# Kernel tuning notes

Hardware: AMD Instinct MI355X
Metric: run time of the kernel (lower is better)

## Reference

```python
import jax, jax.numpy as jnp
import numpy as np

ALPHA = 4.0   # spikingjelly surrogate.Sigmoid default alpha
TAU = 2.0
HEADS = 8

@jax.custom_vjp
def spike_fn(x):
    return (x >= 0).astype(x.dtype)

def _spike_fwd(x):
    return spike_fn(x), x

def _spike_bwd(x, g):
    s = jax.nn.sigmoid(ALPHA * x)
    return (g * ALPHA * s * (1.0 - s),)

spike_fn.defvjp(_spike_fwd, _spike_bwd)

def lif(x, v_th=1.0):
    """Multi-step LIF over leading time axis. Hard reset to 0, detach_reset."""
    def step(v, xt):
        v = v + (xt - v) / TAU
        s = spike_fn(v - v_th)
        v = v * (1.0 - jax.lax.stop_gradient(s))
        return v, s
    _, spikes = jax.lax.scan(step, jnp.zeros_like(x[0]), x)
    return spikes

def conv1x1(x, w, b=None):
    # x: (T,B,C,H,W), w: (O,C) -> (T,B,O,H,W)
    y = jnp.einsum('tbchw,oc->tbohw', x, w)
    if b is not None:
        y = y + b[None, None, :, None, None]
    return y

def bn(x, gamma, beta, mean, var, eps=1e-5):
    inv = gamma / jnp.sqrt(var + eps)
    shift = beta - mean * inv
    return x * inv[None, None, :, None, None] + shift[None, None, :, None, None]

def setup_inputs() -> dict:
    key = jax.random.key(0)
    T, B, C, H, W = 4, 16, 512, 16, 16
    ks = jax.random.split(key, 24)
    def w(k):
        return jax.random.normal(k, (C, C), jnp.float32) * (1.0 / np.sqrt(C))
    def bn_params(k0, k1):
        g = 1.0 + 0.1 * jax.random.normal(k0, (C,), jnp.float32)
        b = 0.1 * jax.random.normal(k1, (C,), jnp.float32)
        m = 0.1 * jax.random.normal(jax.random.fold_in(k0, 7), (C,), jnp.float32)
        v = jax.random.uniform(jax.random.fold_in(k1, 7), (C,), jnp.float32, 0.5, 1.5)
        return g, b, m, v
    x = jax.random.normal(ks[0], (T, B, C, H, W), jnp.float32)
    q_g, q_b, q_m, q_v = bn_params(ks[4], ks[5])
    k_g, k_b, k_m, k_v = bn_params(ks[6], ks[7])
    v_g, v_b, v_m, v_v = bn_params(ks[8], ks[9])
    p_g, p_b2, p_m, p_v = bn_params(ks[10], ks[11])
    return {
        'x': x,
        'q_w': w(ks[1]), 'q_g': q_g, 'q_b': q_b, 'q_m': q_m, 'q_v': q_v,
        'k_w': w(ks[2]), 'k_g': k_g, 'k_b': k_b, 'k_m': k_m, 'k_v': k_v,
        'v_w': w(ks[3]), 'v_g': v_g, 'v_b': v_b, 'v_m': v_m, 'v_v': v_v,
        'proj_w': w(ks[12]),
        'proj_b': 0.1 * jax.random.normal(ks[13], (C,), jnp.float32),
        'p_g': p_g, 'p_b2': p_b2, 'p_m': p_m, 'p_v': p_v,
    }

def reference(x, q_w, q_g, q_b, q_m, q_v, k_w, k_g, k_b, k_m, k_v,
              v_w, v_g, v_b, v_m, v_v, proj_w, proj_b, p_g, p_b2, p_m, p_v):
    T, B, C, H, W = x.shape
    d = C // HEADS
    N = H * W
    identity = x
    xs = lif(x)  # shortcut_lif

    def to_heads(y):
        # (T,B,C,H,W) -> flatten(3) -> (T,B,C,N) -> (T,B,N,C) -> (T,B,N,h,d) -> (T,B,h,N,d)
        return y.reshape(T, B, C, N).transpose(0, 1, 3, 2).reshape(T, B, N, HEADS, d).transpose(0, 1, 3, 2, 4)

    q = to_heads(lif(bn(conv1x1(xs, q_w), q_g, q_b, q_m, q_v)))
    k = to_heads(lif(bn(conv1x1(xs, k_w), k_g, k_b, k_m, k_v)))
    v = to_heads(lif(bn(conv1x1(xs, v_w), v_g, v_b, v_m, v_v)))

    kv = (k * v).sum(axis=3, keepdims=True)        # (T,B,h,1,d) linear spike attention
    kv = lif(kv, v_th=0.5)                         # talking_heads_lif (conv1d never applied in source forward)
    attn = q * kv                                  # (T,B,h,N,d)

    y = attn.transpose(0, 1, 2, 4, 3).reshape(T, B, C, H, W)
    y = bn(conv1x1(y, proj_w, proj_b), p_g, p_b2, p_m, p_v)
    return y + identity
```

## Files before the change

### kernel.cpp

```cpp
#include <hip/hip_runtime.h>


#define T_  4
#define B_  16
#define C_  512
#define N_  256
#define O3_ 1536
#define EPS_ 1e-5f

typedef unsigned int uint32;

__global__ void k0_prep(const float* __restrict__ qw, const float* __restrict__ kw,
                        const float* __restrict__ vw, const float* __restrict__ pw,
                        const float* qg,const float* qb,const float* qm,const float* qv,
                        const float* kg,const float* kb,const float* km,const float* kvr,
                        const float* vg,const float* vb,const float* vm,const float* vv,
                        const float* pg,const float* pb2,const float* pm,const float* pv,
                        const float* projb,
                        float* __restrict__ wqkv_t, float* __restrict__ pwt,
                        float* __restrict__ bnc){
    __shared__ float tile[64 * 65];
    int bx = blockIdx.x, tid = threadIdx.x;
    if (bx < 256) {
        const float* src; float* dst; int ocol;
        int tl;
        if (bx < 192) { int g = bx / 64; tl = bx % 64;
            src = (g == 0) ? qw : (g == 1) ? kw : vw;
            dst = wqkv_t; ocol = g * 512;
        } else { tl = bx - 192; src = pw; dst = pwt; ocol = 0; }
        int o0 = (tl >> 3) * 64, c0 = (tl & 7) * 64;
        int dstride = (bx < 192) ? O3_ : C_;
        #pragma unroll
        for (int i = 0; i < 16; i++) {
            int idx = i * 256 + tid;
            int cl = idx & 63, ol = idx >> 6;
            tile[ol * 65 + cl] = src[(size_t)(o0 + ol) * C_ + c0 + cl];
        }
        __syncthreads();
        #pragma unroll
        for (int i = 0; i < 16; i++) {
            int idx = i * 256 + tid;
            int ol = idx & 63, cl = idx >> 6;
            dst[(size_t)(c0 + cl) * dstride + ocol + o0 + ol] = tile[ol * 65 + cl];
        }
    } else {
        int ch = (bx - 256) * 256 + tid;
        if (ch < C_) {
            {   float inv = qg[ch] / sqrtf(qv[ch] + EPS_);
                bnc[ch] = inv;            bnc[512 + ch]  = qb[ch] - qm[ch] * inv; }
            {   float inv = kg[ch] / sqrtf(kvr[ch] + EPS_);
                bnc[1024 + ch] = inv;     bnc[1536 + ch] = kb[ch] - km[ch] * inv; }
            {   float inv = vg[ch] / sqrtf(vv[ch] + EPS_);
                bnc[2048 + ch] = inv;     bnc[2560 + ch] = vb[ch] - vm[ch] * inv; }
            {   float inv = pg[ch] / sqrtf(pv[ch] + EPS_);
                float shift = pb2[ch] - pm[ch] * inv;
                bnc[3072 + ch] = inv;     bnc[3584 + ch] = projb[ch] * inv + shift; }
        }
    }
}

__global__ void k1_lif_x(const float* __restrict__ x, unsigned char* __restrict__ xs_mask){
    __shared__ unsigned char sm[64 * 68];
    int b = blockIdx.x, c0 = blockIdx.y * 64, n0 = blockIdx.z * 64;
    int tid = threadIdx.x;
    #pragma unroll
    for (int i = 0; i < 16; i++) {
        int idx = i * 256 + tid;
        int nl = idx & 63, cl = idx >> 6;
        const float* xp = x + ((size_t)b * C_ + c0 + cl) * N_ + n0 + nl;
        float v = 0.f; unsigned m = 0;
        #pragma unroll
        for (int t = 0; t < T_; t++) {
            float xt = xp[(size_t)t * B_ * C_ * N_];
            v = v + (xt - v) * 0.5f;
            if (v - 1.0f >= 0.f) { m |= 1u << t; v = 0.f; }
        }
        sm[cl * 68 + nl] = (unsigned char)m;
    }
    __syncthreads();
    #pragma unroll
    for (int i = 0; i < 16; i++) {
        int idx = i * 256 + tid;
        int cl = idx & 63, nl = idx >> 6;
        xs_mask[((size_t)b * N_ + n0 + nl) * C_ + c0 + cl] = sm[cl * 68 + nl];
    }
}

__global__ __launch_bounds__(384) void
k2_qkv(const unsigned char* __restrict__ xs_mask,
       const float* __restrict__ wqkv_t,
       const float* __restrict__ bnc,
       unsigned char* __restrict__ q_mask,
       unsigned char* __restrict__ kvand_mask){
    __shared__ uint32 smask[128];
    __shared__ uint32 scnt;
    __shared__ uint32 slist[512];
    int n = blockIdx.x, b = blockIdx.y, tid = threadIdx.x;
    size_t colbase = ((size_t)b * N_ + n) * C_;
    if (tid < 128) smask[tid] = reinterpret_cast<const uint32*>(xs_mask + colbase)[tid];
    if (tid == 0) scnt = 0;
    __syncthreads();
    if (tid < 256) {
        const unsigned char* smb = (const unsigned char*)smask;
        #pragma unroll
        for (int h = 0; h < 2; h++) {
            int c = tid + (h << 8);
            unsigned m = smb[c];
            if (m) { unsigned p = atomicAdd(&scnt, 1u); slist[p] = (unsigned)c | (m << 16); }
        }
    }
    __syncthreads();
    int cnt = scnt;

    int g = tid >> 7;
    float acc[4][4];
    #pragma unroll
    for (int t = 0; t < 4; t++)
        #pragma unroll
        for (int i = 0; i < 4; i++) acc[t][i] = 0.f;

#define ACC4(t, w_) { acc[t][0]+=w_.x; acc[t][1]+=w_.y; acc[t][2]+=w_.z; acc[t][3]+=w_.w; }
    int j = 0;
    for (; j + 4 <= cnt; j += 4) {
        unsigned e0 = __builtin_amdgcn_readfirstlane(slist[j]);
        unsigned e1 = __builtin_amdgcn_readfirstlane(slist[j + 1]);
        unsigned e2 = __builtin_amdgcn_readfirstlane(slist[j + 2]);
        unsigned e3 = __builtin_amdgcn_readfirstlane(slist[j + 3]);
        float4 w0 = reinterpret_cast<const float4*>(wqkv_t + (size_t)(e0 & 0xffffu) * O3_)[tid];
        float4 w1 = reinterpret_cast<const float4*>(wqkv_t + (size_t)(e1 & 0xffffu) * O3_)[tid];
        float4 w2 = reinterpret_cast<const float4*>(wqkv_t + (size_t)(e2 & 0xffffu) * O3_)[tid];
        float4 w3 = reinterpret_cast<const float4*>(wqkv_t + (size_t)(e3 & 0xffffu) * O3_)[tid];
        unsigned m0 = e0 >> 16, m1 = e1 >> 16, m2 = e2 >> 16, m3 = e3 >> 16;
        if (m0 & 1u) ACC4(0, w0)  if (m0 & 2u) ACC4(1, w0)
        if (m0 & 4u) ACC4(2, w0)  if (m0 & 8u) ACC4(3, w0)
        if (m1 & 1u) ACC4(0, w1)  if (m1 & 2u) ACC4(1, w1)
        if (m1 & 4u) ACC4(2, w1)  if (m1 & 8u) ACC4(3, w1)
        if (m2 & 1u) ACC4(0, w2)  if (m2 & 2u) ACC4(1, w2)
        if (m2 & 4u) ACC4(2, w2)  if (m2 & 8u) ACC4(3, w2)
        if (m3 & 1u) ACC4(0, w3)  if (m3 & 2u) ACC4(1, w3)
        if (m3 & 4u) ACC4(2, w3)  if (m3 & 8u) ACC4(3, w3)
    }
    for (; j < cnt; j++) {
        unsigned e0 = __builtin_amdgcn_readfirstlane(slist[j]);
        float4 w0 = reinterpret_cast<const float4*>(wqkv_t + (size_t)(e0 & 0xffffu) * O3_)[tid];
        unsigned m0 = e0 >> 16;
        if (m0 & 1u) ACC4(0, w0)  if (m0 & 2u) ACC4(1, w0)
        if (m0 & 4u) ACC4(2, w0)  if (m0 & 8u) ACC4(3, w0)
    }
#undef ACC4

    int chb = (tid & 127) * 4;
    unsigned packed = 0;
    #pragma unroll
    for (int i = 0; i < 4; i++) {
        int ch = chb + i;
        float inv = bnc[g * 1024 + ch];
        float sh  = bnc[g * 1024 + 512 + ch];
        float v = 0.f; unsigned bits = 0;
        #pragma unroll
        for (int t = 0; t < 4; t++) {
            float pre = acc[t][i] * inv + sh;
            v = v + (pre - v) * 0.5f;
            if (v - 1.0f >= 0.f) { bits |= 1u << t; v = 0.f; }
        }
        packed |= bits << (8 * i);
    }
    if (g == 0)      reinterpret_cast<uint32*>(q_mask + colbase)[tid] = packed;
    else if (g == 1) smask[tid - 128] = packed;
    __syncthreads();
    if (g == 2) {
        unsigned kb = smask[tid - 256];
        reinterpret_cast<uint32*>(kvand_mask + colbase)[tid - 256] = packed & kb;
    }
}

__global__ void k3_kv(const unsigned char* __restrict__ kvand_mask,
                      unsigned char* __restrict__ kvs_mask){
    int c = blockIdx.x * 256 + threadIdx.x;
    int b = blockIdx.y;
    int cnt[4] = {0, 0, 0, 0};
    const unsigned char* p = kvand_mask + (size_t)b * N_ * C_ + c;
    for (int n = 0; n < N_; n++) {
        unsigned m = p[(size_t)n * C_];
        #pragma unroll
        for (int t = 0; t < 4; t++) cnt[t] += (m >> t) & 1;
    }
    float v = 0.f; unsigned bits = 0;
    #pragma unroll
    for (int t = 0; t < 4; t++) {
        float kvf = (float)cnt[t];
        v = v + (kvf - v) * 0.5f;
        if (v - 0.5f >= 0.f) { bits |= 1u << t; v = 0.f; }
    }
    kvs_mask[b * C_ + c] = (unsigned char)bits;
}

__global__ __launch_bounds__(128) void
k4_attn_proj(const unsigned char* __restrict__ q_mask,
             const unsigned char* __restrict__ kvs_mask,
             const float* __restrict__ pwt,
             const float* __restrict__ bnc,
             float* __restrict__ y_t){
    __shared__ uint32 smask[128];
    __shared__ uint32 scnt;
    __shared__ uint32 slist[512];
    int n = blockIdx.x, b = blockIdx.y, tid = threadIdx.x;
    size_t colbase = ((size_t)b * N_ + n) * C_;
    {
        uint32 qm = reinterpret_cast<const uint32*>(q_mask + colbase)[tid];
        uint32 kv = reinterpret_cast<const uint32*>(kvs_mask + (size_t)b * C_)[tid];
        smask[tid] = qm & kv;
    }
    if (tid == 0) scnt = 0;
    __syncthreads();
    {
        const unsigned char* smb = (const unsigned char*)smask;
        #pragma unroll
        for (int h = 0; h < 4; h++) {
            int c = tid * 4 + h;
            unsigned m = smb[c];
            if (m) { unsigned p = atomicAdd(&scnt, 1u); slist[p] = (unsigned)c | (m << 16); }
        }
    }
    __syncthreads();
    int cnt = scnt;

    float acc[4][4];
    #pragma unroll
    for (int t = 0; t < 4; t++)
        #pragma unroll
        for (int i = 0; i < 4; i++) acc[t][i] = 0.f;

#define ACC4(t, w_) { acc[t][0]+=w_.x; acc[t][1]+=w_.y; acc[t][2]+=w_.z; acc[t][3]+=w_.w; }
    int j = 0;
    for (; j + 4 <= cnt; j += 4) {
        unsigned e0 = __builtin_amdgcn_readfirstlane(slist[j]);
        unsigned e1 = __builtin_amdgcn_readfirstlane(slist[j + 1]);
        unsigned e2 = __builtin_amdgcn_readfirstlane(slist[j + 2]);
        unsigned e3 = __builtin_amdgcn_readfirstlane(slist[j + 3]);
        float4 w0 = reinterpret_cast<const float4*>(pwt + (size_t)(e0 & 0xffffu) * C_)[tid];
        float4 w1 = reinterpret_cast<const float4*>(pwt + (size_t)(e1 & 0xffffu) * C_)[tid];
        float4 w2 = reinterpret_cast<const float4*>(pwt + (size_t)(e2 & 0xffffu) * C_)[tid];
        float4 w3 = reinterpret_cast<const float4*>(pwt + (size_t)(e3 & 0xffffu) * C_)[tid];
        unsigned m0 = e0 >> 16, m1 = e1 >> 16, m2 = e2 >> 16, m3 = e3 >> 16;
        if (m0 & 1u) ACC4(0, w0)  if (m0 & 2u) ACC4(1, w0)
        if (m0 & 4u) ACC4(2, w0)  if (m0 & 8u) ACC4(3, w0)
        if (m1 & 1u) ACC4(0, w1)  if (m1 & 2u) ACC4(1, w1)
        if (m1 & 4u) ACC4(2, w1)  if (m1 & 8u) ACC4(3, w1)
        if (m2 & 1u) ACC4(0, w2)  if (m2 & 2u) ACC4(1, w2)
        if (m2 & 4u) ACC4(2, w2)  if (m2 & 8u) ACC4(3, w2)
        if (m3 & 1u) ACC4(0, w3)  if (m3 & 2u) ACC4(1, w3)
        if (m3 & 4u) ACC4(2, w3)  if (m3 & 8u) ACC4(3, w3)
    }
    for (; j < cnt; j++) {
        unsigned e0 = __builtin_amdgcn_readfirstlane(slist[j]);
        float4 w0 = reinterpret_cast<const float4*>(pwt + (size_t)(e0 & 0xffffu) * C_)[tid];
        unsigned m0 = e0 >> 16;
        if (m0 & 1u) ACC4(0, w0)  if (m0 & 2u) ACC4(1, w0)
        if (m0 & 4u) ACC4(2, w0)  if (m0 & 8u) ACC4(3, w0)
    }
#undef ACC4

    float4 inv = reinterpret_cast<const float4*>(bnc + 3072)[tid];
    float4 sh  = reinterpret_cast<const float4*>(bnc + 3584)[tid];
    #pragma unroll
    for (int t = 0; t < 4; t++) {
        float4 y4;
        y4.x = acc[t][0] * inv.x + sh.x;
        y4.y = acc[t][1] * inv.y + sh.y;
        y4.z = acc[t][2] * inv.z + sh.z;
        y4.w = acc[t][3] * inv.w + sh.w;
        reinterpret_cast<float4*>(y_t + (((size_t)t * B_ + b) * N_ + n) * C_)[tid] = y4;
    }
}

__global__ void k5_out(const float* __restrict__ y_t, const float* __restrict__ x,
                       float* __restrict__ out){
    __shared__ float tile[64 * 65];
    int b = blockIdx.x, o0 = blockIdx.y * 64, n0 = blockIdx.z * 64;
    int tid = threadIdx.x;
    for (int t = 0; t < T_; t++) {
        __syncthreads();
        #pragma unroll
        for (int i = 0; i < 16; i++) {
            int idx = i * 256 + tid;
            int ol = idx & 63, nl = idx >> 6;
            tile[ol * 65 + nl] =
                y_t[(((size_t)t * B_ + b) * N_ + n0 + nl) * C_ + o0 + ol];
        }
        __syncthreads();
        #pragma unroll
        for (int i = 0; i < 16; i++) {
            int idx = i * 256 + tid;
            int nl = idx & 63, ol = idx >> 6;
            size_t a = (((size_t)t * B_ + b) * C_ + o0 + ol) * N_ + n0 + nl;
            out[a] = tile[ol * 65 + nl] + x[a];
        }
    }
}

extern "C" void kernel_launch(void* const* d_in, const int* in_sizes, int n_in,
                              void* d_out, int out_size, void* d_ws, size_t ws_size,
                              hipStream_t stream){
    const float* x     = (const float*)d_in[0];
    const float* q_w   = (const float*)d_in[1];
    const float* q_g   = (const float*)d_in[2];
    const float* q_b   = (const float*)d_in[3];
    const float* q_m   = (const float*)d_in[4];
    const float* q_v   = (const float*)d_in[5];
    const float* k_w   = (const float*)d_in[6];
    const float* k_g   = (const float*)d_in[7];
    const float* k_b   = (const float*)d_in[8];
    const float* k_m   = (const float*)d_in[9];
    const float* k_v   = (const float*)d_in[10];
    const float* v_w   = (const float*)d_in[11];
    const float* v_g   = (const float*)d_in[12];
    const float* v_b   = (const float*)d_in[13];
    const float* v_m   = (const float*)d_in[14];
    const float* v_v   = (const float*)d_in[15];
    const float* pr_w  = (const float*)d_in[16];
    const float* pr_b  = (const float*)d_in[17];
    const float* p_g   = (const float*)d_in[18];
    const float* p_b2  = (const float*)d_in[19];
    const float* p_m   = (const float*)d_in[20];
    const float* p_v   = (const float*)d_in[21];
    float* out = (float*)d_out;

    char* ws = (char*)d_ws;
    float* wqkv_t          = (float*)(ws + 0);
    float* pwt             = (float*)(ws + 3145728);
    float* bnc             = (float*)(ws + 4194304);
    unsigned char* xs_mask = (unsigned char*)(ws + 4210688);
    unsigned char* q_mask  = (unsigned char*)(ws + 6307840);
    unsigned char* kvand   = (unsigned char*)(ws + 8404992);
    unsigned char* kvs     = (unsigned char*)(ws + 10502144);
    float* y_t             = (float*)(ws + 10510336);

    hipLaunchKernelGGL(k0_prep, dim3(258), dim3(256), 0, stream,
                       q_w, k_w, v_w, pr_w,
                       q_g,q_b,q_m,q_v, k_g,k_b,k_m,k_v, v_g,v_b,v_m,v_v,
                       p_g,p_b2,p_m,p_v, pr_b, wqkv_t, pwt, bnc);
    hipLaunchKernelGGL(k1_lif_x, dim3(B_, C_/64, N_/64), dim3(256), 0, stream, x, xs_mask);
    hipLaunchKernelGGL(k2_qkv, dim3(N_, B_), dim3(384), 0, stream,
                       xs_mask, wqkv_t, bnc, q_mask, kvand);
    hipLaunchKernelGGL(k3_kv, dim3(2, B_), dim3(256), 0, stream, kvand, kvs);
    hipLaunchKernelGGL(k4_attn_proj, dim3(N_, B_), dim3(128), 0, stream,
                       q_mask, kvs, pwt, bnc, y_t);
    hipLaunchKernelGGL(k5_out, dim3(B_, C_/64, N_/64), dim3(256), 0, stream, y_t, x, out);
}
```

Baseline: 218.2 us.

## Unroll sparse gathers by 8, SWAR-count kv masks, vectorize output transpose

The sparse weight-gather loops in the QKV and projection kernels are unrolled from 4 to 8 entries, putting more global loads in flight per iteration. The kv reduction kernel now reads 32-bit words and counts four channels at once with SWAR byte lanes, splitting the N dimension across two thread halves combined through shared memory. The output transpose-plus-residual kernel uses float4 global loads and stores. The changes add register pressure in the gather loops and cut k3 to 16 blocks, which leaves very little parallelism.

```diff
diff --git a/kernel.cpp b/kernel.cpp
--- a/kernel.cpp
+++ b/kernel.cpp
@@ -120,33 +120,36 @@
         for (int i = 0; i < 4; i++) acc[t][i] = 0.f;
 
 #define ACC4(t, w_) { acc[t][0]+=w_.x; acc[t][1]+=w_.y; acc[t][2]+=w_.z; acc[t][3]+=w_.w; }
+#define K2MASK(u) { unsigned mm = e##u >> 16; \
+        if (mm & 1u) ACC4(0, w##u)  if (mm & 2u) ACC4(1, w##u) \
+        if (mm & 4u) ACC4(2, w##u)  if (mm & 8u) ACC4(3, w##u) }
     int j = 0;
-    for (; j + 4 <= cnt; j += 4) {
-        unsigned e0 = __builtin_amdgcn_readfirstlane(slist[j]);
+    for (; j + 8 <= cnt; j += 8) {
+        unsigned e0 = __builtin_amdgcn_readfirstlane(slist[j + 0]);
         unsigned e1 = __builtin_amdgcn_readfirstlane(slist[j + 1]);
         unsigned e2 = __builtin_amdgcn_readfirstlane(slist[j + 2]);
         unsigned e3 = __builtin_amdgcn_readfirstlane(slist[j + 3]);
+        unsigned e4 = __builtin_amdgcn_readfirstlane(slist[j + 4]);
+        unsigned e5 = __builtin_amdgcn_readfirstlane(slist[j + 5]);
+        unsigned e6 = __builtin_amdgcn_readfirstlane(slist[j + 6]);
+        unsigned e7 = __builtin_amdgcn_readfirstlane(slist[j + 7]);
         float4 w0 = reinterpret_cast<const float4*>(wqkv_t + (size_t)(e0 & 0xffffu) * O3_)[tid];
         float4 w1 = reinterpret_cast<const float4*>(wqkv_t + (size_t)(e1 & 0xffffu) * O3_)[tid];
         float4 w2 = reinterpret_cast<const float4*>(wqkv_t + (size_t)(e2 & 0xffffu) * O3_)[tid];
         float4 w3 = reinterpret_cast<const float4*>(wqkv_t + (size_t)(e3 & 0xffffu) * O3_)[tid];
-        unsigned m0 = e0 >> 16, m1 = e1 >> 16, m2 = e2 >> 16, m3 = e3 >> 16;
-        if (m0 & 1u) ACC4(0, w0)  if (m0 & 2u) ACC4(1, w0)
-        if (m0 & 4u) ACC4(2, w0)  if (m0 & 8u) ACC4(3, w0)
-        if (m1 & 1u) ACC4(0, w1)  if (m1 & 2u) ACC4(1, w1)
-        if (m1 & 4u) ACC4(2, w1)  if (m1 & 8u) ACC4(3, w1)
-        if (m2 & 1u) ACC4(0, w2)  if (m2 & 2u) ACC4(1, w2)
-        if (m2 & 4u) ACC4(2, w2)  if (m2 & 8u) ACC4(3, w2)
-        if (m3 & 1u) ACC4(0, w3)  if (m3 & 2u) ACC4(1, w3)
-        if (m3 & 4u) ACC4(2, w3)  if (m3 & 8u) ACC4(3, w3)
+        float4 w4 = reinterpret_cast<const float4*>(wqkv_t + (size_t)(e4 & 0xffffu) * O3_)[tid];
+        float4 w5 = reinterpret_cast<const float4*>(wqkv_t + (size_t)(e5 & 0xffffu) * O3_)[tid];
+        float4 w6 = reinterpret_cast<const float4*>(wqkv_t + (size_t)(e6 & 0xffffu) * O3_)[tid];
+        float4 w7 = reinterpret_cast<const float4*>(wqkv_t + (size_t)(e7 & 0xffffu) * O3_)[tid];
+        K2MASK(0) K2MASK(1) K2MASK(2) K2MASK(3)
+        K2MASK(4) K2MASK(5) K2MASK(6) K2MASK(7)
     }
     for (; j < cnt; j++) {
         unsigned e0 = __builtin_amdgcn_readfirstlane(slist[j]);
         float4 w0 = reinterpret_cast<const float4*>(wqkv_t + (size_t)(e0 & 0xffffu) * O3_)[tid];
-        unsigned m0 = e0 >> 16;
-        if (m0 & 1u) ACC4(0, w0)  if (m0 & 2u) ACC4(1, w0)
-        if (m0 & 4u) ACC4(2, w0)  if (m0 & 8u) ACC4(3, w0)
-    }
+        K2MASK(0)
+    }
+#undef K2MASK
 #undef ACC4
 
     int chb = (tid & 127) * 4;
@@ -174,25 +177,43 @@
     }
 }
 
-__global__ void k3_kv(const unsigned char* __restrict__ kvand_mask,
+__global__ void k3_kv(const uint32* __restrict__ kvand32,
                       unsigned char* __restrict__ kvs_mask){
-    int c = blockIdx.x * 256 + threadIdx.x;
-    int b = blockIdx.y;
-    int cnt[4] = {0, 0, 0, 0};
-    const unsigned char* p = kvand_mask + (size_t)b * N_ * C_ + c;
-    for (int n = 0; n < N_; n++) {
-        unsigned m = p[(size_t)n * C_];
-        #pragma unroll
-        for (int t = 0; t < 4; t++) cnt[t] += (m >> t) & 1;
-    }
-    float v = 0.f; unsigned bits = 0;
-    #pragma unroll
-    for (int t = 0; t < 4; t++) {
-        float kvf = (float)cnt[t];
-        v = v + (kvf - v) * 0.5f;
-        if (v - 0.5f >= 0.f) { bits |= 1u << t; v = 0.f; }
-    }
-    kvs_mask[b * C_ + c] = (unsigned char)bits;
+    __shared__ uint32 part[4][128];
+    int b = blockIdx.x, tid = threadIdx.x;
+    int c4 = tid & 127, sub = tid >> 7;
+    const uint32* p = kvand32 + (size_t)b * N_ * 128 + (size_t)sub * 128 * 128 + c4;
+    uint32 cnt0 = 0, cnt1 = 0, cnt2 = 0, cnt3 = 0;
+    for (int i = 0; i < 128; i++) {
+        uint32 m = p[(size_t)i * 128];
+        cnt0 +=  m        & 0x01010101u;
+        cnt1 += (m >> 1)  & 0x01010101u;
+        cnt2 += (m >> 2)  & 0x01010101u;
+        cnt3 += (m >> 3)  & 0x01010101u;
+    }
+    if (sub == 1) { part[0][c4] = cnt0; part[1][c4] = cnt1; part[2][c4] = cnt2; part[3][c4] = cnt3; }
+    __syncthreads();
+    if (sub == 0) {
+        uint32 o0 = part[0][c4], o1 = part[1][c4], o2 = part[2][c4], o3 = part[3][c4];
+        unsigned outp = 0;
+        #pragma unroll
+        for (int e = 0; e < 4; e++) {
+            int sh = 8 * e;
+            float cn[4];
+            cn[0] = (float)(int)(((cnt0 >> sh) & 0xffu) + ((o0 >> sh) & 0xffu));
+            cn[1] = (float)(int)(((cnt1 >> sh) & 0xffu) + ((o1 >> sh) & 0xffu));
+            cn[2] = (float)(int)(((cnt2 >> sh) & 0xffu) + ((o2 >> sh) & 0xffu));
+            cn[3] = (float)(int)(((cnt3 >> sh) & 0xffu) + ((o3 >> sh) & 0xffu));
+            float v = 0.f; unsigned bits = 0;
+            #pragma unroll
+            for (int t = 0; t < 4; t++) {
+                v = v + (cn[t] - v) * 0.5f;
+                if (v - 0.5f >= 0.f) { bits |= 1u << t; v = 0.f; }
+            }
+            outp |= bits << sh;
+        }
+        reinterpret_cast<uint32*>(kvs_mask + (size_t)b * C_)[c4] = outp;
+    }
 }
 
 __global__ __launch_bounds__(128) void
@@ -232,33 +253,36 @@
         for (int i = 0; i < 4; i++) acc[t][i] = 0.f;
 
 #define ACC4(t, w_) { acc[t][0]+=w_.x; acc[t][1]+=w_.y; acc[t][2]+=w_.z; acc[t][3]+=w_.w; }
+#define K4MASK(u) { unsigned mm = e##u >> 16; \
+        if (mm & 1u) ACC4(0, w##u)  if (mm & 2u) ACC4(1, w##u) \
+        if (mm & 4u) ACC4(2, w##u)  if (mm & 8u) ACC4(3, w##u) }
     int j = 0;
-    for (; j + 4 <= cnt; j += 4) {
-        unsigned e0 = __builtin_amdgcn_readfirstlane(slist[j]);
+    for (; j + 8 <= cnt; j += 8) {
+        unsigned e0 = __builtin_amdgcn_readfirstlane(slist[j + 0]);
         unsigned e1 = __builtin_amdgcn_readfirstlane(slist[j + 1]);
         unsigned e2 = __builtin_amdgcn_readfirstlane(slist[j + 2]);
         unsigned e3 = __builtin_amdgcn_readfirstlane(slist[j + 3]);
+        unsigned e4 = __builtin_amdgcn_readfirstlane(slist[j + 4]);
+        unsigned e5 = __builtin_amdgcn_readfirstlane(slist[j + 5]);
+        unsigned e6 = __builtin_amdgcn_readfirstlane(slist[j + 6]);
+        unsigned e7 = __builtin_amdgcn_readfirstlane(slist[j + 7]);
         float4 w0 = reinterpret_cast<const float4*>(pwt + (size_t)(e0 & 0xffffu) * C_)[tid];
         float4 w1 = reinterpret_cast<const float4*>(pwt + (size_t)(e1 & 0xffffu) * C_)[tid];
         float4 w2 = reinterpret_cast<const float4*>(pwt + (size_t)(e2 & 0xffffu) * C_)[tid];
         float4 w3 = reinterpret_cast<const float4*>(pwt + (size_t)(e3 & 0xffffu) * C_)[tid];
-        unsigned m0 = e0 >> 16, m1 = e1 >> 16, m2 = e2 >> 16, m3 = e3 >> 16;
-        if (m0 & 1u) ACC4(0, w0)  if (m0 & 2u) ACC4(1, w0)
-        if (m0 & 4u) ACC4(2, w0)  if (m0 & 8u) ACC4(3, w0)
-        if (m1 & 1u) ACC4(0, w1)  if (m1 & 2u) ACC4(1, w1)
-        if (m1 & 4u) ACC4(2, w1)  if (m1 & 8u) ACC4(3, w1)
-        if (m2 & 1u) ACC4(0, w2)  if (m2 & 2u) ACC4(1, w2)
-        if (m2 & 4u) ACC4(2, w2)  if (m2 & 8u) ACC4(3, w2)
-        if (m3 & 1u) ACC4(0, w3)  if (m3 & 2u) ACC4(1, w3)
-        if (m3 & 4u) ACC4(2, w3)  if (m3 & 8u) ACC4(3, w3)
+        float4 w4 = reinterpret_cast<const float4*>(pwt + (size_t)(e4 & 0xffffu) * C_)[tid];
+        float4 w5 = reinterpret_cast<const float4*>(pwt + (size_t)(e5 & 0xffffu) * C_)[tid];
+        float4 w6 = reinterpret_cast<const float4*>(pwt + (size_t)(e6 & 0xffffu) * C_)[tid];
+        float4 w7 = reinterpret_cast<const float4*>(pwt + (size_t)(e7 & 0xffffu) * C_)[tid];
+        K4MASK(0) K4MASK(1) K4MASK(2) K4MASK(3)
+        K4MASK(4) K4MASK(5) K4MASK(6) K4MASK(7)
     }
     for (; j < cnt; j++) {
         unsigned e0 = __builtin_amdgcn_readfirstlane(slist[j]);
         float4 w0 = reinterpret_cast<const float4*>(pwt + (size_t)(e0 & 0xffffu) * C_)[tid];
-        unsigned m0 = e0 >> 16;
-        if (m0 & 1u) ACC4(0, w0)  if (m0 & 2u) ACC4(1, w0)
-        if (m0 & 4u) ACC4(2, w0)  if (m0 & 8u) ACC4(3, w0)
-    }
+        K4MASK(0)
+    }
+#undef K4MASK
 #undef ACC4
 
     float4 inv = reinterpret_cast<const float4*>(bnc + 3072)[tid];
@@ -282,19 +306,29 @@
     for (int t = 0; t < T_; t++) {
         __syncthreads();
         #pragma unroll
-        for (int i = 0; i < 16; i++) {
+        for (int i = 0; i < 4; i++) {
             int idx = i * 256 + tid;
-            int ol = idx & 63, nl = idx >> 6;
-            tile[ol * 65 + nl] =
-                y_t[(((size_t)t * B_ + b) * N_ + n0 + nl) * C_ + o0 + ol];
+            int o4 = idx & 15, nl = idx >> 4;
+            float4 yv = *reinterpret_cast<const float4*>(
+                y_t + (((size_t)t * B_ + b) * N_ + n0 + nl) * C_ + o0 + o4 * 4);
+            tile[(o4 * 4 + 0) * 65 + nl] = yv.x;
+            tile[(o4 * 4 + 1) * 65 + nl] = yv.y;
+            tile[(o4 * 4 + 2) * 65 + nl] = yv.z;
+            tile[(o4 * 4 + 3) * 65 + nl] = yv.w;
         }
         __syncthreads();
         #pragma unroll
-        for (int i = 0; i < 16; i++) {
+        for (int i = 0; i < 4; i++) {
             int idx = i * 256 + tid;
-            int nl = idx & 63, ol = idx >> 6;
-            size_t a = (((size_t)t * B_ + b) * C_ + o0 + ol) * N_ + n0 + nl;
-            out[a] = tile[ol * 65 + nl] + x[a];
+            int n4 = idx & 15, ol = idx >> 4;
+            size_t a = (((size_t)t * B_ + b) * C_ + o0 + ol) * N_ + n0 + n4 * 4;
+            float4 xv = *reinterpret_cast<const float4*>(x + a);
+            float4 yv;
+            yv.x = tile[ol * 65 + n4 * 4 + 0] + xv.x;
+            yv.y = tile[ol * 65 + n4 * 4 + 1] + xv.y;
+            yv.z = tile[ol * 65 + n4 * 4 + 2] + xv.z;
+            yv.w = tile[ol * 65 + n4 * 4 + 3] + xv.w;
+            *reinterpret_cast<float4*>(out + a) = yv;
         }
     }
 }
@@ -343,7 +377,8 @@
     hipLaunchKernelGGL(k1_lif_x, dim3(B_, C_/64, N_/64), dim3(256), 0, stream, x, xs_mask);
     hipLaunchKernelGGL(k2_qkv, dim3(N_, B_), dim3(384), 0, stream,
                        xs_mask, wqkv_t, bnc, q_mask, kvand);
-    hipLaunchKernelGGL(k3_kv, dim3(2, B_), dim3(256), 0, stream, kvand, kvs);
+    hipLaunchKernelGGL(k3_kv, dim3(B_), dim3(256), 0, stream,
+                       (const uint32*)kvand, kvs);
     hipLaunchKernelGGL(k4_attn_proj, dim3(N_, B_), dim3(128), 0, stream,
                        q_mask, kvs, pwt, bnc, y_t);
     hipLaunchKernelGGL(k5_out, dim3(B_, C_/64, N_/64), dim3(256), 0, stream, y_t, x, out);
```

After: 253.2 us. +16.0%, slower.
